# Kernel optimization log

Hardware: AMD Instinct MI355X
Metric: run time of the kernel (lower is better)

The kernel has to match this reference:

```python
import jax, jax.numpy as jnp
import numpy as np

B, I, J, DIN, DOUT = 256, 1152, 10, 8, 16
ROUTING_ITERS = 3


def squash(v):
    # v: [..., D]; squash(v) = (|v|^2 / (1+|v|^2)) * v/|v| = v * |v| / (1+|v|^2)
    l2 = jnp.linalg.norm(v, axis=-1, keepdims=True)
    return v * (l2 / (1.0 + l2 * l2))


def setup_inputs() -> dict:
    key = jax.random.key(0)
    k1, k2 = jax.random.split(key)
    x = jax.random.normal(k1, (B, I, DIN), dtype=jnp.float32)
    # per-(i,j) Linear(DIN -> DOUT, bias=False) weights, stacked: [I, J, DOUT, DIN]
    W = jax.random.normal(k2, (I, J, DOUT, DIN), dtype=jnp.float32) * 0.1
    return {"x": x, "W": W}


def reference(x, W):
    # prediction vectors u[b,i,j,:] = W[i,j] @ x[b,i,:]  -> [B, I, J, DOUT]
    u = jnp.einsum('bid,ijod->bijo', x, W)
    b = jnp.zeros((I, J), dtype=u.dtype)  # routing logits (shared across batch)
    s = None
    for _ in range(ROUTING_ITERS):
        c = jax.nn.softmax(b, axis=-1)              # [I, J]
        s = jnp.einsum('ij,bijd->bjd', c, u)        # coupling-weighted sum over in-caps
        s = squash(s)                               # [B, J, DOUT]
        # agreement: b[i,j] += sum_b <u[b,i,j], s[b,j]>
        b = b + jnp.einsum('bijd,bjd->ij', u, s)
    return s
```

## Files before the change

### kernel.cpp

```cpp
#include <hip/hip_runtime.h>
#include <math.h>

typedef unsigned short ushort_t;
typedef __attribute__((ext_vector_type(8))) __bf16 bf16x8;
typedef __attribute__((ext_vector_type(4))) float floatx4;

#define B_    256
#define I_    1152
#define J_    10
#define DIN_  8
#define DOUT_ 16
#define K_    (I_*DIN_)
#define N_    (J_*DOUT_)
#define KSPLIT 16
#define KCHUNK (K_/KSPLIT)
#define KSTEPS (KCHUNK/32)

static __device__ __forceinline__ ushort_t f2bf(float f) {
    unsigned int u = __float_as_uint(f);
    u += 0x7fffu + ((u >> 16) & 1u);
    return (ushort_t)(u >> 16);
}
static __device__ __forceinline__ float bf2f(ushort_t h) {
    return __uint_as_float(((unsigned int)h) << 16);
}

__global__ __launch_bounds__(128)
void gemm_s_part_kernel(const float* __restrict__ x, const float* __restrict__ W,
                        const float* __restrict__ blog,
                        float* __restrict__ pbuf, const int iter)
{
    const int tid  = threadIdx.x;
    const int blk  = blockIdx.x;
    const int kb   = blk & 7;
    const int tile = blk >> 3;
    const int mb   = tile & 15;
    const int nt   = tile >> 4;
    const int lane = tid & 63;
    const int w    = tid >> 6;
    const int kc   = kb * 2 + w;

    __shared__ float   c_lds[144];
    __shared__ floatx4 part[2 * 64];

    if (iter > 0) {
        for (int r2 = tid; r2 < 144; r2 += 128) {
            const float* br = blog + (size_t)(kb * 144 + r2) * J_;
            float bv[J_];
            float mx = -1e30f;
            #pragma unroll
            for (int j = 0; j < J_; ++j) { bv[j] = br[j]; mx = fmaxf(mx, bv[j]); }
            float sum = 0.f;
            #pragma unroll
            for (int j = 0; j < J_; ++j) { bv[j] = __expf(bv[j] - mx); sum += bv[j]; }
            c_lds[r2] = bv[nt] / sum;
        }
        __syncthreads();
    }

    {
        const int r = lane & 15, q = lane >> 4;
        const float* ap = x + (size_t)(mb * 16 + r) * K_ + kc * KCHUNK + 8 * q;
        const float* wp = W + (((size_t)(kc * 72 + q) * J_ + nt) * DOUT_ + r) * DIN_;
        const size_t wstep = (size_t)4 * J_ * DOUT_ * DIN_;
        floatx4 acc = {0.f, 0.f, 0.f, 0.f};

        float4 bxa0[2], bxa1[2], bw0[2], bw1[2];
        #pragma unroll
        for (int s = 0; s < 2; ++s) {
            bxa0[s] = *(const float4*)(ap + s * 32);
            bxa1[s] = *(const float4*)(ap + s * 32 + 4);
            bw0[s]  = *(const float4*)(wp + s * wstep);
            bw1[s]  = *(const float4*)(wp + s * wstep + 4);
        }
        #pragma unroll
        for (int s = 0; s < KSTEPS; ++s) {
            float4 xa0 = bxa0[s & 1], xa1 = bxa1[s & 1];
            float4 w0  = bw0[s & 1],  w1  = bw1[s & 1];
            if (s + 2 < KSTEPS) {
                bxa0[s & 1] = *(const float4*)(ap + (s + 2) * 32);
                bxa1[s & 1] = *(const float4*)(ap + (s + 2) * 32 + 4);
                bw0[s & 1]  = *(const float4*)(wp + (s + 2) * wstep);
                bw1[s & 1]  = *(const float4*)(wp + (s + 2) * wstep + 4);
            }
            float cs = (iter == 0) ? 0.1f : c_lds[w * 72 + 4 * s + q];
            float xv[8]  = {xa0.x, xa0.y, xa0.z, xa0.w, xa1.x, xa1.y, xa1.z, xa1.w};
            float wvv[8] = {w0.x, w0.y, w0.z, w0.w, w1.x, w1.y, w1.z, w1.w};
            bf16x8 ah, al, bh, bl;
            #pragma unroll
            for (int e = 0; e < 8; ++e) {
                float xe = xv[e];
                __bf16 h = (__bf16)xe;
                ah[e] = h;
                al[e] = (__bf16)(xe - (float)h);
                float pe = wvv[e] * cs;
                __bf16 g = (__bf16)pe;
                bh[e] = g;
                bl[e] = (__bf16)(pe - (float)g);
            }
            acc = __builtin_amdgcn_mfma_f32_16x16x32_bf16(ah, bh, acc, 0, 0, 0);
            acc = __builtin_amdgcn_mfma_f32_16x16x32_bf16(al, bh, acc, 0, 0, 0);
            acc = __builtin_amdgcn_mfma_f32_16x16x32_bf16(ah, bl, acc, 0, 0, 0);
        }
        part[w * 64 + lane] = acc;
    }
    __syncthreads();

    const int row  = tid >> 3;
    const int col2 = (tid & 7) * 2;
    float2 v2;
    #pragma unroll
    for (int h = 0; h < 2; ++h) {
        const int o      = col2 + h;
        const int lane_c = ((row >> 2) << 4) | o;
        const int reg    = row & 3;
        ((float*)&v2)[h] = part[lane_c][reg] + part[64 + lane_c][reg];
    }
    *(float2*)(pbuf + (size_t)blk * 256 + row * 16 + col2) = v2;
}

__global__ __launch_bounds__(256)
void reduce_squash_kernel(const float* __restrict__ pbuf, float* __restrict__ s_out,
                          ushort_t* __restrict__ Sbt_hi, ushort_t* __restrict__ Sbt_lo,
                          const int iter)
{
    const int tile = blockIdx.x;
    const int mb   = tile & 15;
    const int nt   = tile >> 4;
    const int t    = threadIdx.x;
    const int row  = t >> 4;
    const int o    = t & 15;

    const float* pb = pbuf + (size_t)tile * 8 * 256 + row * 16 + o;
    float v = 0.f;
    #pragma unroll
    for (int u = 0; u < 8; ++u)
        v += pb[u * 256];

    float sq = v * v;
    #pragma unroll
    for (int off = 1; off < 16; off <<= 1)
        sq += __shfl_xor(sq, off, 16);
    float l2 = sqrtf(sq);
    float val = v * (l2 / (1.f + sq));
    const int b  = mb * 16 + row;
    const int jo = nt * 16 + o;
    if (iter == 2) {
        s_out[(size_t)b * N_ + jo] = val;
    } else {
        ushort_t hi = f2bf(val);
        Sbt_hi[(size_t)jo * B_ + b] = hi;
        Sbt_lo[(size_t)jo * B_ + b] = f2bf(val - bf2f(hi));
    }
}

__global__ __launch_bounds__(256)
void gemm_bupd_kernel(const float* __restrict__ x,
                      const ushort_t* __restrict__ Sbt_hi, const ushort_t* __restrict__ Sbt_lo,
                      const float* __restrict__ W, float* __restrict__ blog,
                      const int first)
{
    int wv   = (blockIdx.x & 7) * 360 + (blockIdx.x >> 3) * 4 + (threadIdx.x >> 6);
    int lane = threadIdx.x & 63;
    int mt = wv / 5;
    int jp = wv - mt * 5;
    int j0 = jp * 2, j1 = jp * 2 + 1;
    int r = lane & 15, q = lane >> 4;
    const float* xp = x + (size_t)(8 * q) * K_ + (mt * 16 + r);
    size_t b0off = (size_t)(j0 * 16 + r) * B_ + 8 * q;
    size_t b1off = (size_t)(j1 * 16 + r) * B_ + 8 * q;
    floatx4 acc0 = {0.f, 0.f, 0.f, 0.f};
    floatx4 acc1 = {0.f, 0.f, 0.f, 0.f};

    float xcur[8], xnxt[8];
    #pragma unroll
    for (int e = 0; e < 8; ++e) xcur[e] = xp[(size_t)e * K_];
    #pragma unroll
    for (int s = 0; s < B_ / 32; ++s) {
        if (s + 1 < B_ / 32) {
            #pragma unroll
            for (int e = 0; e < 8; ++e)
                xnxt[e] = xp[(size_t)((s + 1) * 32 + e) * K_];
        }
        bf16x8 ah, al;
        #pragma unroll
        for (int e = 0; e < 8; ++e) {
            float v = xcur[e];
            __bf16 h = (__bf16)v;
            ah[e] = h;
            al[e] = (__bf16)(v - (float)h);
        }
        bf16x8 bh0 = *(const bf16x8*)(Sbt_hi + b0off + s * 32);
        bf16x8 bl0 = *(const bf16x8*)(Sbt_lo + b0off + s * 32);
        bf16x8 bh1 = *(const bf16x8*)(Sbt_hi + b1off + s * 32);
        bf16x8 bl1 = *(const bf16x8*)(Sbt_lo + b1off + s * 32);
        acc0 = __builtin_amdgcn_mfma_f32_16x16x32_bf16(ah, bh0, acc0, 0, 0, 0);
        acc0 = __builtin_amdgcn_mfma_f32_16x16x32_bf16(al, bh0, acc0, 0, 0, 0);
        acc0 = __builtin_amdgcn_mfma_f32_16x16x32_bf16(ah, bl0, acc0, 0, 0, 0);
        acc1 = __builtin_amdgcn_mfma_f32_16x16x32_bf16(ah, bh1, acc1, 0, 0, 0);
        acc1 = __builtin_amdgcn_mfma_f32_16x16x32_bf16(al, bh1, acc1, 0, 0, 0);
        acc1 = __builtin_amdgcn_mfma_f32_16x16x32_bf16(ah, bl1, acc1, 0, 0, 0);
        #pragma unroll
        for (int e = 0; e < 8; ++e) xcur[e] = xnxt[e];
    }
    int i  = mt * 2 + (q >> 1);
    int d0 = (q & 1) * 4;
    int o  = lane & 15;
    int iw = mt * 2 + (lane >> 5);
    {
        const float4 w4 = *(const float4*)(W + ((((size_t)i * J_ + j0) * DOUT_ + o) * DIN_ + d0));
        float val = acc0[0] * w4.x + acc0[1] * w4.y + acc0[2] * w4.z + acc0[3] * w4.w;
        #pragma unroll
        for (int off = 1; off < 32; off <<= 1)
            val += __shfl_xor(val, off, 32);
        if ((lane & 31) == 0) {
            float* dst = blog + (size_t)iw * J_ + j0;
            if (first) *dst = val; else *dst += val;
        }
    }
    {
        const float4 w4 = *(const float4*)(W + ((((size_t)i * J_ + j1) * DOUT_ + o) * DIN_ + d0));
        float val = acc1[0] * w4.x + acc1[1] * w4.y + acc1[2] * w4.z + acc1[3] * w4.w;
        #pragma unroll
        for (int off = 1; off < 32; off <<= 1)
            val += __shfl_xor(val, off, 32);
        if ((lane & 31) == 0) {
            float* dst = blog + (size_t)iw * J_ + j1;
            if (first) *dst = val; else *dst += val;
        }
    }
}

extern "C" void kernel_launch(void* const* d_in, const int* in_sizes, int n_in,
                              void* d_out, int out_size, void* d_ws, size_t ws_size,
                              hipStream_t stream)
{
    const float* x = (const float*)d_in[0];
    const float* W = (const float*)d_in[1];
    float* s_out = (float*)d_out;

    char* ws = (char*)d_ws;
    ushort_t* Sbt_hi = (ushort_t*)(ws);
    ushort_t* Sbt_lo = (ushort_t*)(ws + 81920);
    float*    blog   = (float*)   (ws + 163840);
    float*    pbuf   = (float*)   (ws + 262144);

    for (int it = 0; it < 3; ++it) {
        gemm_s_part_kernel<<<1280, 128, 0, stream>>>(x, W, blog, pbuf, it);
        reduce_squash_kernel<<<160, 256, 0, stream>>>(pbuf, s_out,
                                                      Sbt_hi, Sbt_lo, it);
        if (it < 2)
            gemm_bupd_kernel<<<720, 256, 0, stream>>>(x, Sbt_hi, Sbt_lo,
                                                      W, blog, it == 0 ? 1 : 0);
    }
}
```

Baseline: 141.7 us.

## Prepack x as split bf16 and W into lane-contiguous layout for s-GEMM

Adds two prep kernels that run once per call. The first splits x into hi/lo bf16 pairs and the second reorders W, both into a layout where each lane of the s-GEMM reads contiguous 16-byte vectors. The gemm_s_part kernel then loads pre-split x directly and no longer repeats the bf16 split three times per iteration, and its W loads become coalesced. This costs two extra launches and extra workspace traffic, and the bupd kernel still reads the original x and W.

```diff
diff --git a/kernel.cpp b/kernel.cpp
--- a/kernel.cpp
+++ b/kernel.cpp
@@ -16,6 +16,8 @@
 #define KCHUNK (K_/KSPLIT)
 #define KSTEPS (KCHUNK/32)
 
+#define CHUNK16 2368
+
 static __device__ __forceinline__ ushort_t f2bf(float f) {
     unsigned int u = __float_as_uint(f);
     u += 0x7fffu + ((u >> 16) & 1u);
@@ -25,8 +27,53 @@
     return __uint_as_float(((unsigned int)h) << 16);
 }
 
+__global__ __launch_bounds__(256)
+void prep_xpack_kernel(const float* __restrict__ x, ushort_t* __restrict__ xPk)
+{
+    const int gid = blockIdx.x * 256 + threadIdx.x;
+    const int f   = gid * 8;
+    const int row = f / K_;
+    const int kk  = f - row * K_;
+    const int kc  = kk / KCHUNK;
+    const int t   = kk - kc * KCHUNK;
+    const int s   = t >> 5;
+    const int q   = (t & 31) >> 3;
+    const int mb  = row >> 4, r = row & 15;
+
+    const float* src = x + (size_t)f;
+    bf16x8 h8, l8;
+    #pragma unroll
+    for (int e = 0; e < 8; ++e) {
+        float v = src[e];
+        __bf16 h = (__bf16)v;
+        h8[e] = h;
+        l8[e] = (__bf16)(v - (float)h);
+    }
+    bf16x8* dst = (bf16x8*)xPk + (size_t)(mb * 16 + kc) * CHUNK16 + s * 128 + q * 16 + r;
+    dst[0]  = h8;
+    dst[64] = l8;
+}
+
+__global__ __launch_bounds__(256)
+void prep_wpack_kernel(const float* __restrict__ W, float* __restrict__ wPk)
+{
+    const int gid = blockIdx.x * 256 + threadIdx.x;
+    const int f   = gid * 4;
+    const int i   = f / 1280;
+    const int rem = f - i * 1280;
+    const int no  = rem >> 3;
+    const int p   = (rem >> 2) & 1;
+    const int nt  = no >> 4, r = no & 15;
+    const int kc  = i / 72;
+    const int m   = i - kc * 72;
+    const int s   = m >> 2, q = m & 3;
+
+    float4 v = *(const float4*)(W + (size_t)f);
+    ((float4*)wPk)[(size_t)(nt * 16 + kc) * CHUNK16 + (s * 2 + p) * 64 + q * 16 + r] = v;
+}
+
 __global__ __launch_bounds__(128)
-void gemm_s_part_kernel(const float* __restrict__ x, const float* __restrict__ W,
+void gemm_s_part_kernel(const ushort_t* __restrict__ xPk, const float* __restrict__ wPk,
                         const float* __restrict__ blog,
                         float* __restrict__ pbuf, const int iter)
 {
@@ -59,40 +106,35 @@
     }
 
     {
-        const int r = lane & 15, q = lane >> 4;
-        const float* ap = x + (size_t)(mb * 16 + r) * K_ + kc * KCHUNK + 8 * q;
-        const float* wp = W + (((size_t)(kc * 72 + q) * J_ + nt) * DOUT_ + r) * DIN_;
-        const size_t wstep = (size_t)4 * J_ * DOUT_ * DIN_;
+        const int q = lane >> 4;
+        const bf16x8* xp = (const bf16x8*)xPk + (size_t)(mb * 16 + kc) * CHUNK16 + lane;
+        const float4* wp = (const float4*)wPk + (size_t)(nt * 16 + kc) * CHUNK16 + lane;
         floatx4 acc = {0.f, 0.f, 0.f, 0.f};
 
-        float4 bxa0[2], bxa1[2], bw0[2], bw1[2];
+        bf16x8 rah[2], ral[2];
+        float4 rw0[2], rw1[2];
         #pragma unroll
         for (int s = 0; s < 2; ++s) {
-            bxa0[s] = *(const float4*)(ap + s * 32);
-            bxa1[s] = *(const float4*)(ap + s * 32 + 4);
-            bw0[s]  = *(const float4*)(wp + s * wstep);
-            bw1[s]  = *(const float4*)(wp + s * wstep + 4);
+            rah[s] = xp[s * 128];
+            ral[s] = xp[s * 128 + 64];
+            rw0[s] = wp[s * 128];
+            rw1[s] = wp[s * 128 + 64];
         }
         #pragma unroll
         for (int s = 0; s < KSTEPS; ++s) {
-            float4 xa0 = bxa0[s & 1], xa1 = bxa1[s & 1];
-            float4 w0  = bw0[s & 1],  w1  = bw1[s & 1];
+            bf16x8 ah = rah[s & 1], al = ral[s & 1];
+            float4 w0 = rw0[s & 1], w1 = rw1[s & 1];
             if (s + 2 < KSTEPS) {
-                bxa0[s & 1] = *(const float4*)(ap + (s + 2) * 32);
-                bxa1[s & 1] = *(const float4*)(ap + (s + 2) * 32 + 4);
-                bw0[s & 1]  = *(const float4*)(wp + (s + 2) * wstep);
-                bw1[s & 1]  = *(const float4*)(wp + (s + 2) * wstep + 4);
+                rah[s & 1] = xp[(s + 2) * 128];
+                ral[s & 1] = xp[(s + 2) * 128 + 64];
+                rw0[s & 1] = wp[(s + 2) * 128];
+                rw1[s & 1] = wp[(s + 2) * 128 + 64];
             }
             float cs = (iter == 0) ? 0.1f : c_lds[w * 72 + 4 * s + q];
-            float xv[8]  = {xa0.x, xa0.y, xa0.z, xa0.w, xa1.x, xa1.y, xa1.z, xa1.w};
             float wvv[8] = {w0.x, w0.y, w0.z, w0.w, w1.x, w1.y, w1.z, w1.w};
-            bf16x8 ah, al, bh, bl;
+            bf16x8 bh, bl;
             #pragma unroll
             for (int e = 0; e < 8; ++e) {
-                float xe = xv[e];
-                __bf16 h = (__bf16)xe;
-                ah[e] = h;
-                al[e] = (__bf16)(xe - (float)h);
                 float pe = wvv[e] * cs;
                 __bf16 g = (__bf16)pe;
                 bh[e] = g;
@@ -244,9 +286,14 @@
     ushort_t* Sbt_lo = (ushort_t*)(ws + 81920);
     float*    blog   = (float*)   (ws + 163840);
     float*    pbuf   = (float*)   (ws + 262144);
+    ushort_t* xPk    = (ushort_t*)(ws + 1572864);
+    float*    wPk    = (float*)   (ws + 11272192);
+
+    prep_xpack_kernel<<<1152, 256, 0, stream>>>(x, xPk);
+    prep_wpack_kernel<<<1440, 256, 0, stream>>>(W, wPk);
 
     for (int it = 0; it < 3; ++it) {
-        gemm_s_part_kernel<<<1280, 128, 0, stream>>>(x, W, blog, pbuf, it);
+        gemm_s_part_kernel<<<1280, 128, 0, stream>>>(xPk, wPk, blog, pbuf, it);
         reduce_squash_kernel<<<160, 256, 0, stream>>>(pbuf, s_out,
                                                       Sbt_hi, Sbt_lo, it);
         if (it < 2)
```

After: 135.9 us. 4.0% less time.
